# Performance work log

Hardware: AMD Instinct MI355X
Metric: run time of the kernel (lower is better)

## Reference

```python
import jax, jax.numpy as jnp
import numpy as np

B, S, H, M = 8, 128, 768, 128
EPS = 1e-12


def setup_inputs() -> dict:
    key = jax.random.key(0)
    ks = jax.random.split(key, 8)
    seq_hiddens = jax.random.normal(ks[0], (B, S, H), dtype=jnp.float32)
    gamma = jnp.ones((H,), jnp.float32)
    beta = jnp.zeros((H,), jnp.float32)
    # conditional LN dense weights (torch Linear weight: (out, in)); small init so math stays stable
    w_beta = jax.random.normal(ks[1], (H, H), dtype=jnp.float32) * 0.02
    w_gamma = jax.random.normal(ks[2], (H, H), dtype=jnp.float32) * 0.02
    w_ent = jax.random.normal(ks[3], (H, M), dtype=jnp.float32) * 0.02
    w_head = jax.random.normal(ks[4], (H, M), dtype=jnp.float32) * 0.02
    w_tail = jax.random.normal(ks[5], (H, M), dtype=jnp.float32) * 0.02
    b_ent = jnp.zeros((M,), jnp.float32)
    b_head = jnp.zeros((M,), jnp.float32)
    b_tail = jnp.zeros((M,), jnp.float32)
    return dict(seq_hiddens=seq_hiddens, gamma=gamma, beta=beta, w_beta=w_beta,
                w_gamma=w_gamma, w_ent=w_ent, b_ent=b_ent, w_head=w_head,
                b_head=b_head, w_tail=w_tail, b_tail=b_tail)


def _handshake_cln(seq, gamma, beta, w_beta, w_gamma):
    # Triangular pair expansion in the same row-major order as the torch loop:
    # for ind in range(S): pairs (ind, ind), (ind, ind+1), ..., (ind, S-1)
    s = seq.shape[1]
    ii, jj = jnp.triu_indices(s)                 # (P,) each, P = S(S+1)/2
    x = seq[:, jj, :]                            # visible hiddens   (B, P, H)
    cond = seq[:, ii, :]                         # repeated hiddens  (B, P, H)
    beta_c = jnp.einsum('bph,oh->bpo', cond, w_beta) + beta      # (B, P, H)
    gamma_c = jnp.einsum('bph,oh->bpo', cond, w_gamma) + gamma   # (B, P, H)
    mean = jnp.mean(x, axis=-1, keepdims=True)
    out = x - mean
    var = jnp.mean(out * out, axis=-1, keepdims=True)
    std = (var + EPS) ** 2                       # NOTE: faithful to source (no sqrt)
    return out / std * gamma_c + beta_c


def reference(seq_hiddens, gamma, beta, w_beta, w_gamma, w_ent, b_ent,
              w_head, b_head, w_tail, b_tail):
    shaking = _handshake_cln(seq_hiddens, gamma, beta, w_beta, w_gamma)  # (B, P, H)
    ent = jnp.tanh(shaking @ w_ent + b_ent)      # (B, P, M)
    head = jnp.tanh(shaking @ w_head + b_head)
    tail = jnp.tanh(shaking @ w_tail + b_tail)
    return jnp.stack([ent, head, tail], axis=0)  # (3, B, P, M)
```

## Files before the change

kernel.cpp:

```cpp
#include <hip/hip_runtime.h>
#include <hip/hip_bf16.h>
#include <hip/hip_fp16.h>
#include <math.h>

#define B_   8
#define S_   128
#define H_   768
#define M_   128
#define P_   8256
#define BP_  66048
#define EPSF 1e-12f

typedef unsigned short u16;
typedef unsigned int   u32;
typedef _Float16 h16;
typedef _Float16 ffrag __attribute__((ext_vector_type(8)));
typedef float    f32x4 __attribute__((ext_vector_type(4)));

__device__ __forceinline__ u32 fuse2(u32 x, u32 g, u32 b) {
    __half2 r = __hfma2(__builtin_bit_cast(__half2, x),
                        __builtin_bit_cast(__half2, g),
                        __builtin_bit_cast(__half2, b));
    return __builtin_bit_cast(u32, r);
}
__device__ __forceinline__ float fast_tanh(float v) {
    float t = __expf(v + v);
    float r = __builtin_amdgcn_rcpf(t + 1.0f);
    return fmaf(-2.0f, r, 1.0f);
}
__device__ __forceinline__ void gl_lds16(const h16* g, h16* l) {
    __builtin_amdgcn_global_load_lds(
        (const __attribute__((address_space(1))) u32*)g,
        (__attribute__((address_space(3))) u32*)l, 16, 0, 0);
}

#define NORM0 5763
__global__ void k_prep(const float* __restrict__ seq,
                       const float* __restrict__ wg, const float* __restrict__ wb,
                       const float* __restrict__ we, const float* __restrict__ wh,
                       const float* __restrict__ wt,
                       const float* __restrict__ be, const float* __restrict__ bh,
                       const float* __restrict__ bt,
                       h16* __restrict__ wgb, h16* __restrict__ wbb,
                       h16* __restrict__ wpk, float* __restrict__ biasc,
                       h16* __restrict__ xn, h16* __restrict__ condb)
{
    __shared__ float red[4];
    const int bx = blockIdx.x;
    const int t = threadIdx.x;

    if (bx < NORM0) {
        int idx = bx * 256 + t;
        if (idx < 589824) {
            wgb[idx] = (h16)wg[idx];
        } else if (idx < 1179648) {
            int i = idx - 589824;
            wbb[i] = (h16)wb[i];
        } else if (idx < 1474560) {
            int i = idx - 1179648;
            int e  = i & 7;
            int u  = i >> 3;
            int n  = u % 192;
            int v  = u / 192;
            int ch = v & 7;
            int w2 = v >> 3;
            int kt = w2 % 12;
            int nb = w2 / 12;
            int h  = kt * 64 + ch * 8 + e;
            int ng = nb * 192 + n;
            int head = ng >> 7, m = ng & 127;
            const float* src = (head == 0) ? we : (head == 1 ? wh : wt);
            wpk[i] = (h16)src[h * 128 + m];
        } else if (idx < 1474944) {
            int n = idx - 1474560;
            biasc[n] = (n < 128) ? be[n] : (n < 256 ? bh[n - 128] : bt[n - 256]);
        }
        return;
    }
    const int row = bx - NORM0;
    const int lane = t & 63, wid = t >> 6;
    const float* x = seq + (size_t)row * H_;
    float x0 = x[t], x1 = x[t + 256], x2 = x[t + 512];

    float s = x0 + x1 + x2;
    for (int o = 32; o; o >>= 1) s += __shfl_xor(s, o);
    if (lane == 0) red[wid] = s;
    __syncthreads();
    float mean = (red[0] + red[1] + red[2] + red[3]) * (1.0f / 768.0f);

    float c0 = x0 - mean, c1 = x1 - mean, c2 = x2 - mean;
    float ss = c0 * c0 + c1 * c1 + c2 * c2;
    for (int o = 32; o; o >>= 1) ss += __shfl_xor(ss, o);
    __syncthreads();
    if (lane == 0) red[wid] = ss;
    __syncthreads();
    float var = (red[0] + red[1] + red[2] + red[3]) * (1.0f / 768.0f);
    float sd = var + EPSF;
    float scale = 1.0f / (sd * sd);

    h16* xr = xn + (size_t)row * H_;
    h16* cr = condb + (size_t)row * H_;
    xr[t] = (h16)(c0 * scale); xr[t + 256] = (h16)(c1 * scale); xr[t + 512] = (h16)(c2 * scale);
    cr[t] = (h16)x0;           cr[t + 256] = (h16)x1;           cr[t + 512] = (h16)x2;
}

__global__ __launch_bounds__(256) void k_cond_gemm(
    const h16* __restrict__ Ab, const h16* __restrict__ Wg, const h16* __restrict__ Wb,
    const float* __restrict__ gamma, const float* __restrict__ beta,
    h16* __restrict__ Gc, h16* __restrict__ Bc)
{
    __shared__ h16 Ash[64 * 72];
    __shared__ h16 Bsh[64 * 72];
    const int t = threadIdx.x;
    const int row0 = blockIdx.x * 64;
    const int by = blockIdx.y;
    const bool isg = (by < 12);
    const int nc0 = (isg ? by : by - 12) * 64;
    const h16* wsrc = isg ? Wg : Wb;

    const int r = t >> 2, q = t & 3;
    const h16* ap = Ab + (size_t)(row0 + r) * H_ + q * 16;
    const h16* wp = wsrc + (size_t)(nc0 + r) * H_ + q * 16;
    h16* asto = &Ash[r * 72 + q * 16];
    h16* bsto = &Bsh[r * 72 + q * 16];

    const int lane = t & 63, wid = t >> 6;
    const int wm0 = (wid >> 1) * 32, wn0 = (wid & 1) * 32;
    const int l15 = lane & 15, quad = lane >> 4, q8 = quad * 8;

    f32x4 acc[2][2] = {};
    for (int kt = 0; kt < 12; ++kt) {
        const int k0 = kt * 64;
        uint4 a0 = *(const uint4*)(ap + k0); uint4 a1 = *(const uint4*)(ap + k0 + 8);
        uint4 w0 = *(const uint4*)(wp + k0); uint4 w1 = *(const uint4*)(wp + k0 + 8);
        *(uint4*)asto = a0; *(uint4*)(asto + 8) = a1;
        *(uint4*)bsto = w0; *(uint4*)(bsto + 8) = w1;
        __syncthreads();
#pragma unroll
        for (int ks = 0; ks < 64; ks += 32) {
            ffrag af[2], bf[2];
#pragma unroll
            for (int mi = 0; mi < 2; ++mi)
                af[mi] = *reinterpret_cast<const ffrag*>(&Ash[(wm0 + mi * 16 + l15) * 72 + ks + q8]);
#pragma unroll
            for (int ni = 0; ni < 2; ++ni)
                bf[ni] = *reinterpret_cast<const ffrag*>(&Bsh[(wn0 + ni * 16 + l15) * 72 + ks + q8]);
#pragma unroll
            for (int mi = 0; mi < 2; ++mi)
#pragma unroll
                for (int ni = 0; ni < 2; ++ni)
                    acc[mi][ni] = __builtin_amdgcn_mfma_f32_16x16x32_f16(af[mi], bf[ni], acc[mi][ni], 0, 0, 0);
        }
        __syncthreads();
    }

    const float* bias = isg ? gamma : beta;
    h16* outp = isg ? Gc : Bc;
#pragma unroll
    for (int mi = 0; mi < 2; ++mi)
#pragma unroll
        for (int ni = 0; ni < 2; ++ni) {
            int c = wn0 + ni * 16 + l15;
            float bv = bias[nc0 + c];
#pragma unroll
            for (int reg = 0; reg < 4; ++reg) {
                int rg = wm0 + mi * 16 + quad * 4 + reg;
                outp[(size_t)(row0 + rg) * H_ + nc0 + c] = (h16)(acc[mi][ni][reg] + bv);
            }
        }
}

__global__ __launch_bounds__(256, 2) void k_pair_gemm(
    const h16* __restrict__ Xn, const h16* __restrict__ Gcb, const h16* __restrict__ Bcb,
    const h16* __restrict__ Wpk, const float* __restrict__ biasc,
    float* __restrict__ out)
{
    __shared__ h16 Ash[2][8 * 64 * 8];
    __shared__ h16 Bsh[2][8 * 192 * 8];
    __shared__ int offx[64];
    __shared__ int offc[64];

    const int t = threadIdx.x;
    const int row0 = blockIdx.x * 64;
    const int nb = blockIdx.y;

    if (t < 64) {
        int gp = row0 + t;
        int b = gp / P_;
        int p = gp - b * P_;
        int i = (int)((257.0f - sqrtf(66049.0f - 8.0f * (float)p)) * 0.5f);
        if (i < 0) i = 0; if (i > 127) i = 127;
        while (i > 0 && (i * (257 - i)) / 2 > p) --i;
        while (((i + 1) * (256 - i)) / 2 <= p) ++i;
        int j = i + (p - (i * (257 - i)) / 2);
        offx[t] = b * 128 + j;
        offc[t] = b * 128 + i;
    }
    __syncthreads();

    const int r = t >> 2, c4 = t & 3;
    const h16* xp  = Xn  + (size_t)offx[r] * H_ + c4 * 16;
    const h16* gp_ = Gcb + (size_t)offc[r] * H_ + c4 * 16;
    const h16* bp_ = Bcb + (size_t)offc[r] * H_ + c4 * 16;
    const int aw0 = ((2 * c4) * 64 + r) * 8;
    const int aw1 = ((2 * c4 + 1) * 64 + r) * 8;

    const h16* wtile = Wpk + (size_t)nb * 12 * 12288;
    const int wud = t & ~63;

    const int lane = t & 63, wid = t >> 6;
    const int wn0 = wid * 48;
    const int l15 = lane & 15, quad = lane >> 4;

#pragma unroll
    for (int c = 0; c < 6; ++c)
        gl_lds16(wtile + (size_t)(c * 256 + t) * 8, &Bsh[0][(c * 256 + wud) * 8]);
    {
        uint4 xa = *(const uint4*)xp;   uint4 xb = *(const uint4*)(xp + 8);
        uint4 ga = *(const uint4*)gp_;  uint4 gb = *(const uint4*)(gp_ + 8);
        uint4 ba = *(const uint4*)bp_;  uint4 bb = *(const uint4*)(bp_ + 8);
        uint4 f0, f1;
        f0.x = fuse2(xa.x, ga.x, ba.x); f0.y = fuse2(xa.y, ga.y, ba.y);
        f0.z = fuse2(xa.z, ga.z, ba.z); f0.w = fuse2(xa.w, ga.w, ba.w);
        f1.x = fuse2(xb.x, gb.x, bb.x); f1.y = fuse2(xb.y, gb.y, bb.y);
        f1.z = fuse2(xb.z, gb.z, bb.z); f1.w = fuse2(xb.w, gb.w, bb.w);
        *(uint4*)&Ash[0][aw0] = f0; *(uint4*)&Ash[0][aw1] = f1;
    }
    __syncthreads();

    f32x4 acc[4][3] = {};
#pragma unroll 2
    for (int kt = 0; kt < 12; ++kt) {
        const int buf = kt & 1, nbf = buf ^ 1;
        uint4 xa, xb, ga, gb, ba, bb;
        if (kt < 11) {
            const h16* wnext = wtile + (size_t)(kt + 1) * 12288;
#pragma unroll
            for (int c = 0; c < 6; ++c)
                gl_lds16(wnext + (size_t)(c * 256 + t) * 8, &Bsh[nbf][(c * 256 + wud) * 8]);
            const int k0 = (kt + 1) * 64;
            xa = *(const uint4*)(xp + k0);  xb = *(const uint4*)(xp + k0 + 8);
            ga = *(const uint4*)(gp_ + k0); gb = *(const uint4*)(gp_ + k0 + 8);
            ba = *(const uint4*)(bp_ + k0); bb = *(const uint4*)(bp_ + k0 + 8);
        }

#pragma unroll
        for (int ks = 0; ks < 64; ks += 32) {
            const int ch0 = ks >> 3;
            ffrag af[4], bf[3];
#pragma unroll
            for (int mi = 0; mi < 4; ++mi)
                af[mi] = *reinterpret_cast<const ffrag*>(
                    &Ash[buf][((ch0 + quad) * 64 + mi * 16 + l15) * 8]);
#pragma unroll
            for (int ni = 0; ni < 3; ++ni)
                bf[ni] = *reinterpret_cast<const ffrag*>(
                    &Bsh[buf][((ch0 + quad) * 192 + wn0 + ni * 16 + l15) * 8]);
#pragma unroll
            for (int mi = 0; mi < 4; ++mi)
#pragma unroll
                for (int ni = 0; ni < 3; ++ni)
                    acc[mi][ni] = __builtin_amdgcn_mfma_f32_16x16x32_f16(af[mi], bf[ni], acc[mi][ni], 0, 0, 0);
        }

        if (kt < 11) {
            uint4 f0, f1;
            f0.x = fuse2(xa.x, ga.x, ba.x); f0.y = fuse2(xa.y, ga.y, ba.y);
            f0.z = fuse2(xa.z, ga.z, ba.z); f0.w = fuse2(xa.w, ga.w, ba.w);
            f1.x = fuse2(xb.x, gb.x, bb.x); f1.y = fuse2(xb.y, gb.y, bb.y);
            f1.z = fuse2(xb.z, gb.z, bb.z); f1.w = fuse2(xb.w, gb.w, bb.w);
            *(uint4*)&Ash[nbf][aw0] = f0; *(uint4*)&Ash[nbf][aw1] = f1;
        }
        __syncthreads();
    }

#pragma unroll
    for (int mi = 0; mi < 4; ++mi)
#pragma unroll
        for (int ni = 0; ni < 3; ++ni) {
            int cg = nb * 192 + wn0 + ni * 16 + l15;
            int head = cg >> 7, m = cg & 127;
            float bv = biasc[cg];
#pragma unroll
            for (int reg = 0; reg < 4; ++reg) {
                int rg = mi * 16 + quad * 4 + reg;
                out[((size_t)head * BP_ + row0 + rg) * M_ + m] = fast_tanh(acc[mi][ni][reg] + bv);
            }
        }
}

extern "C" void kernel_launch(void* const* d_in, const int* in_sizes, int n_in,
                              void* d_out, int out_size, void* d_ws, size_t ws_size,
                              hipStream_t stream)
{
    const float* seq     = (const float*)d_in[0];
    const float* gamma   = (const float*)d_in[1];
    const float* beta    = (const float*)d_in[2];
    const float* w_beta  = (const float*)d_in[3];
    const float* w_gamma = (const float*)d_in[4];
    const float* w_ent   = (const float*)d_in[5];
    const float* b_ent   = (const float*)d_in[6];
    const float* w_head  = (const float*)d_in[7];
    const float* b_head  = (const float*)d_in[8];
    const float* w_tail  = (const float*)d_in[9];
    const float* b_tail  = (const float*)d_in[10];
    float* out = (float*)d_out;

    char* ws = (char*)d_ws;
    h16* xn    = (h16*)ws; ws += (size_t)1024 * 768 * 2;
    h16* condb = (h16*)ws; ws += (size_t)1024 * 768 * 2;
    h16* wgb   = (h16*)ws; ws += (size_t)768 * 768 * 2;
    h16* wbb   = (h16*)ws; ws += (size_t)768 * 768 * 2;
    h16* wpk   = (h16*)ws; ws += (size_t)294912 * 2;
    h16* gc    = (h16*)ws; ws += (size_t)1024 * 768 * 2;
    h16* bc    = (h16*)ws; ws += (size_t)1024 * 768 * 2;
    float* biasc = (float*)ws; ws += 384 * 4;

    hipLaunchKernelGGL(k_prep, dim3(NORM0 + 1024), dim3(256), 0, stream,
                       seq, w_gamma, w_beta, w_ent, w_head, w_tail,
                       b_ent, b_head, b_tail, wgb, wbb, wpk, biasc, xn, condb);
    hipLaunchKernelGGL(k_cond_gemm, dim3(16, 24), dim3(256), 0, stream,
                       condb, wgb, wbb, gamma, beta, gc, bc);
    hipLaunchKernelGGL(k_pair_gemm, dim3(1032, 2), dim3(256), 0, stream,
                       xn, gc, bc, wpk, biasc, out);
}
```

Before: 212.6 us.

## Retile pair GEMM to 128x128 blocks with one head per block column

The pair GEMM moves from 64x192 tiles (2 column blocks) to 128x128 tiles (3 column blocks, one per output head). The weight packing changes to match, each wave now computes a 64x64 sub-tile, and every thread computes its own row's triangular indices instead of using shared offset tables. The aim is to cut how often the fused A operand (x*gamma+beta) is rebuilt per output column and to raise MFMA work per LDS load. The cost is more accumulator registers per thread and more redundant fused-A building, since each A row is now rebuilt in 3 column blocks instead of 2.

Result: faster. 200.5 us (-5.7%).

```diff
diff --git a/kernel.cpp b/kernel.cpp
--- a/kernel.cpp
+++ b/kernel.cpp
@@ -59,18 +59,15 @@
         } else if (idx < 1474560) {
             int i = idx - 1179648;
             int e  = i & 7;
-            int u  = i >> 3;
-            int n  = u % 192;
-            int v  = u / 192;
+            int n  = (i >> 3) & 127;
+            int v  = i >> 10;
             int ch = v & 7;
             int w2 = v >> 3;
             int kt = w2 % 12;
             int nb = w2 / 12;
             int h  = kt * 64 + ch * 8 + e;
-            int ng = nb * 192 + n;
-            int head = ng >> 7, m = ng & 127;
-            const float* src = (head == 0) ? we : (head == 1 ? wh : wt);
-            wpk[i] = (h16)src[h * 128 + m];
+            const float* src = (nb == 0) ? we : (nb == 1 ? wh : wt);
+            wpk[i] = (h16)src[h * 128 + n];
         } else if (idx < 1474944) {
             int n = idx - 1474560;
             biasc[n] = (n < 128) ? be[n] : (n < 256 ? bh[n - 128] : bt[n - 256]);
@@ -175,101 +172,105 @@
     const h16* __restrict__ Wpk, const float* __restrict__ biasc,
     float* __restrict__ out)
 {
-    __shared__ h16 Ash[2][8 * 64 * 8];
-    __shared__ h16 Bsh[2][8 * 192 * 8];
-    __shared__ int offx[64];
-    __shared__ int offc[64];
+    __shared__ h16 Ash[2][8 * 128 * 8];
+    __shared__ h16 Bsh[2][8 * 128 * 8];
 
     const int t = threadIdx.x;
-    const int row0 = blockIdx.x * 64;
+    const int row0 = blockIdx.x * 128;
     const int nb = blockIdx.y;
 
-    if (t < 64) {
-        int gp = row0 + t;
-        int b = gp / P_;
-        int p = gp - b * P_;
-        int i = (int)((257.0f - sqrtf(66049.0f - 8.0f * (float)p)) * 0.5f);
-        if (i < 0) i = 0; if (i > 127) i = 127;
-        while (i > 0 && (i * (257 - i)) / 2 > p) --i;
-        while (((i + 1) * (256 - i)) / 2 <= p) ++i;
-        int j = i + (p - (i * (257 - i)) / 2);
-        offx[t] = b * 128 + j;
-        offc[t] = b * 128 + i;
+    const int r_s = t >> 1, half = t & 1;
+    int gp = row0 + r_s;
+    int b = gp / P_;
+    int p = gp - b * P_;
+    int i = (int)((257.0f - sqrtf(66049.0f - 8.0f * (float)p)) * 0.5f);
+    if (i < 0) i = 0; if (i > 127) i = 127;
+    while (i > 0 && (i * (257 - i)) / 2 > p) --i;
+    while (((i + 1) * (256 - i)) / 2 <= p) ++i;
+    int j = i + (p - (i * (257 - i)) / 2);
+
+    const h16* xp  = Xn  + (size_t)(b * 128 + j) * H_ + half * 32;
+    const h16* gp_ = Gcb + (size_t)(b * 128 + i) * H_ + half * 32;
+    const h16* bp_ = Bcb + (size_t)(b * 128 + i) * H_ + half * 32;
+    int aw[4];
+#pragma unroll
+    for (int u = 0; u < 4; ++u)
+        aw[u] = ((half * 4 + u) * 128 + r_s) * 8;
+
+    const h16* wtile = Wpk + (size_t)nb * 12 * 8192;
+    const int wud = t & ~63;
+
+    const int lane = t & 63, wid = t >> 6;
+    const int wm0 = (wid >> 1) * 64, wn0 = (wid & 1) * 64;
+    const int l15 = lane & 15, quad = lane >> 4;
+
+#pragma unroll
+    for (int c = 0; c < 4; ++c)
+        gl_lds16(wtile + (size_t)(c * 256 + t) * 8, &Bsh[0][(c * 256 + wud) * 8]);
+    {
+        uint4 xa[4], ga[4], ba[4];
+#pragma unroll
+        for (int u = 0; u < 4; ++u) {
+            xa[u] = *(const uint4*)(xp + u * 8);
+            ga[u] = *(const uint4*)(gp_ + u * 8);
+            ba[u] = *(const uint4*)(bp_ + u * 8);
+        }
+#pragma unroll
+        for (int u = 0; u < 4; ++u) {
+            uint4 f;
+            f.x = fuse2(xa[u].x, ga[u].x, ba[u].x); f.y = fuse2(xa[u].y, ga[u].y, ba[u].y);
+            f.z = fuse2(xa[u].z, ga[u].z, ba[u].z); f.w = fuse2(xa[u].w, ga[u].w, ba[u].w);
+            *(uint4*)&Ash[0][aw[u]] = f;
+        }
     }
     __syncthreads();
 
-    const int r = t >> 2, c4 = t & 3;
-    const h16* xp  = Xn  + (size_t)offx[r] * H_ + c4 * 16;
-    const h16* gp_ = Gcb + (size_t)offc[r] * H_ + c4 * 16;
-    const h16* bp_ = Bcb + (size_t)offc[r] * H_ + c4 * 16;
-    const int aw0 = ((2 * c4) * 64 + r) * 8;
-    const int aw1 = ((2 * c4 + 1) * 64 + r) * 8;
-
-    const h16* wtile = Wpk + (size_t)nb * 12 * 12288;
-    const int wud = t & ~63;
-
-    const int lane = t & 63, wid = t >> 6;
-    const int wn0 = wid * 48;
-    const int l15 = lane & 15, quad = lane >> 4;
-
-#pragma unroll
-    for (int c = 0; c < 6; ++c)
-        gl_lds16(wtile + (size_t)(c * 256 + t) * 8, &Bsh[0][(c * 256 + wud) * 8]);
-    {
-        uint4 xa = *(const uint4*)xp;   uint4 xb = *(const uint4*)(xp + 8);
-        uint4 ga = *(const uint4*)gp_;  uint4 gb = *(const uint4*)(gp_ + 8);
-        uint4 ba = *(const uint4*)bp_;  uint4 bb = *(const uint4*)(bp_ + 8);
-        uint4 f0, f1;
-        f0.x = fuse2(xa.x, ga.x, ba.x); f0.y = fuse2(xa.y, ga.y, ba.y);
-        f0.z = fuse2(xa.z, ga.z, ba.z); f0.w = fuse2(xa.w, ga.w, ba.w);
-        f1.x = fuse2(xb.x, gb.x, bb.x); f1.y = fuse2(xb.y, gb.y, bb.y);
-        f1.z = fuse2(xb.z, gb.z, bb.z); f1.w = fuse2(xb.w, gb.w, bb.w);
-        *(uint4*)&Ash[0][aw0] = f0; *(uint4*)&Ash[0][aw1] = f1;
-    }
-    __syncthreads();
-
-    f32x4 acc[4][3] = {};
+    f32x4 acc[4][4] = {};
 #pragma unroll 2
     for (int kt = 0; kt < 12; ++kt) {
         const int buf = kt & 1, nbf = buf ^ 1;
-        uint4 xa, xb, ga, gb, ba, bb;
+        uint4 xa[4], ga[4], ba[4];
         if (kt < 11) {
-            const h16* wnext = wtile + (size_t)(kt + 1) * 12288;
-#pragma unroll
-            for (int c = 0; c < 6; ++c)
+            const h16* wnext = wtile + (size_t)(kt + 1) * 8192;
+#pragma unroll
+            for (int c = 0; c < 4; ++c)
                 gl_lds16(wnext + (size_t)(c * 256 + t) * 8, &Bsh[nbf][(c * 256 + wud) * 8]);
             const int k0 = (kt + 1) * 64;
-            xa = *(const uint4*)(xp + k0);  xb = *(const uint4*)(xp + k0 + 8);
-            ga = *(const uint4*)(gp_ + k0); gb = *(const uint4*)(gp_ + k0 + 8);
-            ba = *(const uint4*)(bp_ + k0); bb = *(const uint4*)(bp_ + k0 + 8);
+#pragma unroll
+            for (int u = 0; u < 4; ++u) {
+                xa[u] = *(const uint4*)(xp + k0 + u * 8);
+                ga[u] = *(const uint4*)(gp_ + k0 + u * 8);
+                ba[u] = *(const uint4*)(bp_ + k0 + u * 8);
+            }
         }
 
 #pragma unroll
         for (int ks = 0; ks < 64; ks += 32) {
             const int ch0 = ks >> 3;
-            ffrag af[4], bf[3];
+            ffrag af[4], bf[4];
 #pragma unroll
             for (int mi = 0; mi < 4; ++mi)
                 af[mi] = *reinterpret_cast<const ffrag*>(
-                    &Ash[buf][((ch0 + quad) * 64 + mi * 16 + l15) * 8]);
-#pragma unroll
-            for (int ni = 0; ni < 3; ++ni)
+                    &Ash[buf][((ch0 + quad) * 128 + wm0 + mi * 16 + l15) * 8]);
+#pragma unroll
+            for (int ni = 0; ni < 4; ++ni)
                 bf[ni] = *reinterpret_cast<const ffrag*>(
-                    &Bsh[buf][((ch0 + quad) * 192 + wn0 + ni * 16 + l15) * 8]);
+                    &Bsh[buf][((ch0 + quad) * 128 + wn0 + ni * 16 + l15) * 8]);
 #pragma unroll
             for (int mi = 0; mi < 4; ++mi)
 #pragma unroll
-                for (int ni = 0; ni < 3; ++ni)
+                for (int ni = 0; ni < 4; ++ni)
                     acc[mi][ni] = __builtin_amdgcn_mfma_f32_16x16x32_f16(af[mi], bf[ni], acc[mi][ni], 0, 0, 0);
         }
 
         if (kt < 11) {
-            uint4 f0, f1;
-            f0.x = fuse2(xa.x, ga.x, ba.x); f0.y = fuse2(xa.y, ga.y, ba.y);
-            f0.z = fuse2(xa.z, ga.z, ba.z); f0.w = fuse2(xa.w, ga.w, ba.w);
-            f1.x = fuse2(xb.x, gb.x, bb.x); f1.y = fuse2(xb.y, gb.y, bb.y);
-            f1.z = fuse2(xb.z, gb.z, bb.z); f1.w = fuse2(xb.w, gb.w, bb.w);
-            *(uint4*)&Ash[nbf][aw0] = f0; *(uint4*)&Ash[nbf][aw1] = f1;
+#pragma unroll
+            for (int u = 0; u < 4; ++u) {
+                uint4 f;
+                f.x = fuse2(xa[u].x, ga[u].x, ba[u].x); f.y = fuse2(xa[u].y, ga[u].y, ba[u].y);
+                f.z = fuse2(xa[u].z, ga[u].z, ba[u].z); f.w = fuse2(xa[u].w, ga[u].w, ba[u].w);
+                *(uint4*)&Ash[nbf][aw[u]] = f;
+            }
         }
         __syncthreads();
     }
@@ -277,14 +278,13 @@
 #pragma unroll
     for (int mi = 0; mi < 4; ++mi)
 #pragma unroll
-        for (int ni = 0; ni < 3; ++ni) {
-            int cg = nb * 192 + wn0 + ni * 16 + l15;
-            int head = cg >> 7, m = cg & 127;
-            float bv = biasc[cg];
+        for (int ni = 0; ni < 4; ++ni) {
+            int c = wn0 + ni * 16 + l15;
+            float bv = biasc[nb * 128 + c];
 #pragma unroll
             for (int reg = 0; reg < 4; ++reg) {
-                int rg = mi * 16 + quad * 4 + reg;
-                out[((size_t)head * BP_ + row0 + rg) * M_ + m] = fast_tanh(acc[mi][ni][reg] + bv);
+                int rg = wm0 + mi * 16 + quad * 4 + reg;
+                out[((size_t)nb * BP_ + row0 + rg) * M_ + c] = fast_tanh(acc[mi][ni][reg] + bv);
             }
         }
 }
@@ -321,6 +321,6 @@
                        b_ent, b_head, b_tail, wgb, wbb, wpk, biasc, xn, condb);
     hipLaunchKernelGGL(k_cond_gemm, dim3(16, 24), dim3(256), 0, stream,
                        condb, wgb, wbb, gamma, beta, gc, bc);
-    hipLaunchKernelGGL(k_pair_gemm, dim3(1032, 2), dim3(256), 0, stream,
+    hipLaunchKernelGGL(k_pair_gemm, dim3(516, 3), dim3(256), 0, stream,
                        xn, gc, bc, wpk, biasc, out);
 }
```
